# Optimization experiments

Measured on AMD Instinct MI355X. Metric: run time of the kernel, lower is better.

Reference implementation:

```python
import jax, jax.numpy as jnp
import numpy as np
import math

DIM = 2048
NUM_HEADS = 16
HEAD_DIM = DIM // NUM_HEADS
SEQ = 2048
BATCH = 4
THETA = 10000.0


def _rope_tables(seq_len, d, theta):
    # faithful to RotaryEmbedding: emb = cat([freqs, freqs], -1), then [..., ::2]
    inv_freq = 1.0 / theta ** (np.arange(0, d, 2, dtype=np.float32) / d)  # [d/2]
    t = np.arange(seq_len, dtype=np.float32)
    freqs = np.einsum('i,j->ij', t, inv_freq)          # [S, d/2]
    emb = np.concatenate([freqs, freqs], axis=-1)       # [S, d]
    cos_split = np.cos(emb)[:, ::2]                     # [S, d/2]
    sin_split = np.sin(emb)[:, ::2]                     # [S, d/2]
    return jnp.asarray(cos_split), jnp.asarray(sin_split)


def _apply_rope(x, cos_s, sin_s):
    # x: [b, h, s, d]; cos_s/sin_s: [s, d/2]
    x1 = x[..., ::2]
    x2 = x[..., 1::2]
    c = cos_s[None, None]
    s = sin_s[None, None]
    return jnp.concatenate([x1 * c - x2 * s, x1 * s + x2 * c], axis=-1)


def setup_inputs() -> dict:
    key = jax.random.key(0)
    k1, k2, k3 = jax.random.split(key, 3)
    x = jax.random.normal(k1, (BATCH, SEQ, DIM), dtype=jnp.float32)
    # causal additive mask [1,1,S,S]
    neg = jnp.finfo(jnp.float32).min
    causal = jnp.tril(jnp.ones((SEQ, SEQ), dtype=bool))
    mask = jnp.where(causal, 0.0, neg)[None, None].astype(jnp.float32)
    w_qkv = jax.random.normal(k2, (3 * DIM, DIM), dtype=jnp.float32) * (1.0 / math.sqrt(DIM))
    w_out = jax.random.normal(k3, (DIM, DIM), dtype=jnp.float32) * (1.0 / math.sqrt(DIM))
    return {"x": x, "mask": mask, "w_qkv": w_qkv, "w_out": w_out}


def reference(x, mask, w_qkv, w_out):
    b, s, _ = x.shape
    h, d = NUM_HEADS, HEAD_DIM
    qkv = jnp.einsum('bse,fe->bsf', x, w_qkv)           # [b, s, 3*dim]
    q, k, v = jnp.split(qkv, 3, axis=-1)
    # b s (h d) -> b h s d
    reshp = lambda t: t.reshape(b, s, h, d).transpose(0, 2, 1, 3)
    q, k, v = reshp(q), reshp(k), reshp(v)
    cos_s, sin_s = _rope_tables(s, d, THETA)
    q = _apply_rope(q, cos_s, sin_s)
    k = _apply_rope(k, cos_s, sin_s)
    att = jnp.einsum('bhqd,bhkd->bhqk', q, k) / math.sqrt(d)
    att = att + mask
    att = jax.nn.softmax(att, axis=-1)
    y = jnp.einsum('bhqk,bhkd->bhqd', att, v)           # [b, h, s, d]
    y = y.transpose(0, 2, 1, 3).reshape(b, s, h * d)
    return jnp.einsum('bse,fe->bsf', y, w_out)
```

## Files before the change

kernel.cpp:

```cpp
#include <hip/hip_runtime.h>

typedef unsigned short u16;
typedef unsigned int u32;
typedef __attribute__((ext_vector_type(4))) float f32x4;
typedef __attribute__((ext_vector_type(16))) float f32x16;
typedef __attribute__((ext_vector_type(8))) short bf16x8;
typedef __attribute__((ext_vector_type(4))) float float4v;
typedef __attribute__((ext_vector_type(4))) unsigned short u16x4;
typedef __attribute__((ext_vector_type(8))) unsigned short u16x8;

__device__ __forceinline__ float bf2f(u16 u) { return __uint_as_float(((u32)u) << 16); }
__device__ __forceinline__ u16 f2bf(float f) {
  u32 x = __float_as_uint(f);
  x += 0x7fffu + ((x >> 16) & 1u);
  return (u16)(x >> 16);
}
__device__ __forceinline__ u32 cvtpk(float lo, float hi_) {
  u32 r;
  asm("v_cvt_pk_bf16_f32 %0, %1, %2" : "=v"(r) : "v"(lo), "v"(hi_));
  return r;
}

__device__ __forceinline__ void gll16(const void* g, void* l) {
  __builtin_amdgcn_global_load_lds((const __attribute__((address_space(1))) void*)g,
                                   (__attribute__((address_space(3))) void*)l, 16, 0, 0);
}

#define MFMA_BF16(a, b, c) __builtin_amdgcn_mfma_f32_16x16x32_bf16((a), (b), (c), 0, 0, 0)
#define MFMA32(a, b, c) __builtin_amdgcn_mfma_f32_32x32x16_bf16((a), (b), (c), 0, 0, 0)

#define BARRIER() __builtin_amdgcn_s_barrier()
#define SETP(n) __builtin_amdgcn_s_setprio(n)
#define VMCNT(n) asm volatile("s_waitcnt vmcnt(" #n ")" ::: "memory")

__global__ __launch_bounds__(256) void prep_kernel(const float* __restrict__ x,
                                                   const float* __restrict__ w_qkv,
                                                   const float* __restrict__ w_out,
                                                   u16* __restrict__ xb,
                                                   u16* __restrict__ wqkvb,
                                                   u16* __restrict__ woutb,
                                                   float2* __restrict__ cst) {
  const int tid0 = blockIdx.x * 256 + threadIdx.x;
  const int stride = gridDim.x * 256;
#pragma unroll 1
  for (int i = tid0 * 4; i < 16777216; i += stride * 4) {
    const float4v v = *(const float4v*)(x + i);
    u16x4 o; o[0] = f2bf(v[0]); o[1] = f2bf(v[1]); o[2] = f2bf(v[2]); o[3] = f2bf(v[3]);
    *(u16x4*)(xb + i) = o;
  }
#pragma unroll 1
  for (int i = tid0 * 4; i < 12582912; i += stride * 4) {
    const float4v v = *(const float4v*)(w_qkv + i);
    u16x4 o; o[0] = f2bf(v[0]); o[1] = f2bf(v[1]); o[2] = f2bf(v[2]); o[3] = f2bf(v[3]);
    *(u16x4*)(wqkvb + i) = o;
  }
#pragma unroll 1
  for (int i = tid0 * 4; i < 4194304; i += stride * 4) {
    const float4v v = *(const float4v*)(w_out + i);
    u16x4 o; o[0] = f2bf(v[0]); o[1] = f2bf(v[1]); o[2] = f2bf(v[2]); o[3] = f2bf(v[3]);
    *(u16x4*)(woutb + i) = o;
  }
#pragma unroll 1
  for (int idx = tid0; idx < 131072; idx += stride) {
    const int t = idx >> 6, j = idx & 63;
    const float inv = powf(10000.0f, -(float)(j & 31) * (1.0f / 32.0f));
    const float ang = (float)t * inv;
    cst[idx] = make_float2(cosf(ang), sinf(ang));
  }
}

#define PH_MFMA(MG, NG, BF)                                                      \
  do {                                                                           \
    _Pragma("unroll") for (int i_ = 0; i_ < 4; ++i_)                             \
      _Pragma("unroll") for (int jn_ = 0; jn_ < 2; ++jn_)                        \
        _Pragma("unroll") for (int ks_ = 0; ks_ < 2; ++ks_)                      \
          acc[(MG) * 4 + i_][(NG) * 2 + jn_] =                                   \
              MFMA_BF16(af[i_][ks_], BF[jn_][ks_],                               \
                        acc[(MG) * 4 + i_][(NG) * 2 + jn_]);                     \
  } while (0)

#define LDB_M(bb, ng, BF)                                                        \
  do {                                                                           \
    const char* base_ = (const char*)&LDS[bb][1][ng][0];                         \
    _Pragma("unroll") for (int jn_ = 0; jn_ < 2; ++jn_) {                        \
      const int R_ = jn_ * 64 + wc * 16 + l15;                                   \
      _Pragma("unroll") for (int ks_ = 0; ks_ < 2; ++ks_)                        \
        BF[jn_][ks_] = *(const bf16x8*)(base_ + R_ * 128 +                       \
                                        ((ks_ * 64 + l4 * 16) ^ ((R_ & 7) << 4)));\
    }                                                                            \
  } while (0)

#define KTILE(BB, OB, TT)                                                        \
  do {                                                                           \
    LDA_(BB, 0); LDB_M(BB, 0, bfr0);                                            \
    if ((TT) + 1 < NT) STAGE(OB, 0, 0, (TT) + 1);                                \
    BARRIER(); SETP(1); PH_MFMA(0, 0, bfr0); SETP(0); BARRIER();                 \
    LDB_M(BB, 1, bfr1);                                                          \
    if ((TT) + 2 < NT) STAGE(BB, 1, 0, (TT) + 2);                                \
    BARRIER(); SETP(1); PH_MFMA(0, 1, bfr1); SETP(0); BARRIER();                 \
    LDA_(BB, 1);                                                                 \
    if ((TT) + 2 < NT) STAGE(BB, 1, 1, (TT) + 2);                                \
    BARRIER(); SETP(1); PH_MFMA(1, 1, bfr1); SETP(0); BARRIER();                 \
    if ((TT) + 2 < NT) STAGE(BB, 0, 1, (TT) + 2);                                \
    BARRIER(); SETP(1); PH_MFMA(1, 0, bfr0); SETP(0);                            \
    if ((TT) + 2 < NT) { VMCNT(6); } else { VMCNT(0); }                          \
    BARRIER();                                                                   \
  } while (0)

template <int MODE>
__global__ __launch_bounds__(512, 2) void gemm_bt8(const u16* __restrict__ A,
                                                   const u16* __restrict__ B,
                                                   void* __restrict__ Cv, int M, int N, int K,
                                                   int lda, int ldb, int ldc,
                                                   const float2* __restrict__ cst) {
  __shared__ __align__(16) u16 LDS[2][2][2][128 * 64];
  const int nbn = N >> 8;
  const int nwg = gridDim.x;
  const int wg = (blockIdx.x & 7) * (nwg >> 3) + (blockIdx.x >> 3);
  const int bm = wg / nbn, bn = wg % nbn;
  const int tid = threadIdx.x;
  const int w = tid >> 6, l = tid & 63, l15 = l & 15, l4 = l >> 4;
  const int wr = w >> 2, wc = w & 3;
  const u16* Abase = A + (size_t)bm * 256 * lda;
  const u16* Bbase = B + (size_t)bn * 256 * ldb;
  const int NT = K >> 6;

  f32x4 acc[8][4] = {};
  bf16x8 af[4][2], bfr0[2][2], bfr1[2][2];

  auto STAGE = [&](int buf, int sel, int h, int t) {
    const u16* src = (sel ? Bbase + (size_t)h * 128 * ldb : Abase + (size_t)h * 128 * lda) +
                     t * 64;
    const int ld = sel ? ldb : lda;
    char* dst = (char*)&LDS[buf][sel][h][0];
#pragma unroll
    for (int j = 0; j < 2; ++j) {
      const int o = j * 8192 + tid * 16;
      const int r = o >> 7;
      const int cb = (o & 127) ^ ((r & 7) << 4);
      gll16(src + (size_t)r * ld + (cb >> 1), dst + o);
    }
  };
  auto LDA_ = [&](int bb, int mg) {
    const char* base = (const char*)&LDS[bb][0][mg][0];
#pragma unroll
    for (int i = 0; i < 4; ++i) {
      const int R = i * 32 + wr * 16 + l15;
#pragma unroll
      for (int ks = 0; ks < 2; ++ks)
        af[i][ks] = *(const bf16x8*)(base + R * 128 + ((ks * 64 + l4 * 16) ^ ((R & 7) << 4)));
    }
  };

  STAGE(0, 0, 0, 0); STAGE(0, 1, 0, 0); STAGE(0, 0, 1, 0); STAGE(0, 1, 1, 0);
  STAGE(1, 1, 0, 1); STAGE(1, 1, 1, 1); STAGE(1, 0, 1, 1);
  VMCNT(6);
  BARRIER();

  for (int T = 0; T < NT; T += 2) {
    KTILE(0, 1, T);
    KTILE(1, 0, T + 1);
  }

#pragma unroll
  for (int mf = 0; mf < 8; ++mf) {
    const int mg = mf >> 2, i = mf & 3;
    const int row0 = bm * 256 + mg * 128 + i * 32 + wr * 16 + l4 * 4;
#pragma unroll
    for (int f = 0; f < 4; ++f) {
      const int col = bn * 256 + f * 64 + wc * 16 + l15;
      const f32x4 a = acc[mf][f];
      if (MODE == 0) {
        float* C = (float*)Cv;
#pragma unroll
        for (int r = 0; r < 4; ++r)
          C[(size_t)(row0 + r) * ldc + col] = a[r];
      } else if (bn < 16) {
        u16* C = (u16*)Cv;
        const int hc = (f * 64 + wc * 16 + l15) & 127;
        const int jj = hc >> 1;
        const int odd = hc & 1;
        const int co = (col & ~127) + jj + (odd << 6);
#pragma unroll
        for (int r = 0; r < 4; ++r) {
          const int row = row0 + r;
          const int seq = row & 2047;
          const float v = a[r];
          const float p = __shfl_xor(v, 1);
          const float2 cv = cst[seq * 64 + jj];
          const float res = odd ? (p * cv.y + v * cv.x)
                                : (v * cv.x - p * cv.y);
          C[(size_t)row * 6144 + co] = f2bf(res);
        }
      } else {
        u16* C = (u16*)Cv;
        const int batch = row0 >> 11;
        const int s0 = row0 & 2047;
        const int vcol = col - 4096;
        u16* vb = C + (size_t)((batch * 16 + (vcol >> 7)) * 128 + (vcol & 127)) * 6144 +
                  4096 + s0;
        union { u32 u[2]; u16x4 v; } pk;
        pk.u[0] = cvtpk(a[0], a[1]);
        pk.u[1] = cvtpk(a[2], a[3]);
        *(u16x4*)vb = pk.v;
      }
    }
  }
}

__global__ __launch_bounds__(512, 2) void flash_attn(u16* __restrict__ qkvb) {
  __shared__ __align__(16) char smem[65536];
  const int bh = blockIdx.x;
  const int qt = 7 - blockIdx.y;
  const int b = bh >> 4, h = bh & 15;
  const int tid = threadIdx.x;
  const int w = tid >> 6, l = tid & 63;
  const int l31 = l & 31, hi = l >> 5;

  const int q0 = qt * 256 + w * 32;
  const int qg = q0 + l31;

  bf16x8 qf[8];
  {
    const u16* Qrow = qkvb + (size_t)(b * 2048 + qg) * 6144 + h * 128 + hi * 8;
#pragma unroll
    for (int d = 0; d < 8; ++d) qf[d] = *(const bf16x8*)(Qrow + d * 16);
  }

  f32x16 ot[4];
#pragma unroll
  for (int dt = 0; dt < 4; ++dt) ot[dt] = 0.f;
  float mrun = -1e30f, lrun = 0.f;

  const int NT = 4 * qt + 4;
  const u16* Kg0 = qkvb + (size_t)b * 2048 * 6144 + 2048 + h * 128;
  const u16* Vg0 = qkvb + (size_t)bh * 128 * 6144 + 4096;

  auto STAGE = [&](int t) {
    const u16* Kg = Kg0 + (size_t)t * 64 * 6144;
    const u16* Vg = Vg0 + t * 64;
    char* kd = smem + (t & 1) * 16384;
    char* vd = smem + 32768 + (t & 1) * 16384;
#pragma unroll
    for (int j = 0; j < 2; ++j) {
      const int o = j * 8192 + tid * 16;
      {
        const int r = o >> 8;
        const int cb = (o & 255) ^ ((r & 15) << 4);
        gll16(Kg + (size_t)r * 6144 + (cb >> 1), kd + o);
      }
      {
        const int r = o >> 7;
        const int cb = (o & 127) ^ ((r & 7) << 4);
        gll16(Vg + (size_t)r * 6144 + (cb >> 1), vd + o);
      }
    }
  };

  STAGE(0);
  VMCNT(0);
  BARRIER();

  for (int kt = 0; kt < NT; ++kt) {
    if (kt + 1 < NT) STAGE(kt + 1);

    if (kt * 64 <= q0 + 31) {
      const char* Kb = smem + (kt & 1) * 16384;
      const char* Vb = smem + 32768 + (kt & 1) * 16384;

      f32x16 sa[2];
      sa[0] = 0.f; sa[1] = 0.f;
#pragma unroll
      for (int ks2 = 0; ks2 < 2; ++ks2) {
        const int R = ks2 * 32 + l31;
#pragma unroll
        for (int d = 0; d < 8; ++d) {
          const bf16x8 kf = *(const bf16x8*)(Kb + R * 256 +
                                             ((d * 32 + hi * 16) ^ ((R & 15) << 4)));
          sa[ks2] = MFMA32(kf, qf[d], sa[ks2]);
        }
      }

      const float SCALE = 0.08838834764831845f;
      float tmax = -1e30f;
      if (kt * 64 + 63 > q0) {
#pragma unroll
        for (int ks2 = 0; ks2 < 2; ++ks2)
#pragma unroll
          for (int rg = 0; rg < 16; ++rg) {
            const int key = kt * 64 + ks2 * 32 + (rg & 3) + 8 * (rg >> 2) + 4 * hi;
            float sv = sa[ks2][rg] * SCALE;
            sv = (key > qg) ? -1e30f : sv;
            sa[ks2][rg] = sv;
            tmax = fmaxf(tmax, sv);
          }
      } else {
#pragma unroll
        for (int ks2 = 0; ks2 < 2; ++ks2)
#pragma unroll
          for (int rg = 0; rg < 16; ++rg) {
            const float sv = sa[ks2][rg] * SCALE;
            sa[ks2][rg] = sv;
            tmax = fmaxf(tmax, sv);
          }
      }
      tmax = fmaxf(tmax, __shfl_xor(tmax, 32));

      const float mnew = fmaxf(mrun, tmax);
      const float alpha = __expf(mrun - mnew);
      mrun = mnew;
      float rsum = 0.f;
#pragma unroll
      for (int ks2 = 0; ks2 < 2; ++ks2)
#pragma unroll
        for (int rg = 0; rg < 16; ++rg) {
          const float pv = __expf(sa[ks2][rg] - mnew);
          sa[ks2][rg] = pv;
          rsum += pv;
        }
      rsum += __shfl_xor(rsum, 32);
      lrun = lrun * alpha + rsum;
#pragma unroll
      for (int dt = 0; dt < 4; ++dt)
#pragma unroll
        for (int rg = 0; rg < 16; ++rg) ot[dt][rg] *= alpha;

      bf16x8 pfrag[4];
#pragma unroll
      for (int t = 0; t < 4; ++t) {
        const int ks2 = t >> 1;
        const int gA = 2 * (t & 1);
        const int gB = gA + 1;
        const u32 a0 = cvtpk(sa[ks2][gA * 4 + 0], sa[ks2][gA * 4 + 1]);
        const u32 a1 = cvtpk(sa[ks2][gA * 4 + 2], sa[ks2][gA * 4 + 3]);
        const u32 b0 = cvtpk(sa[ks2][gB * 4 + 0], sa[ks2][gB * 4 + 1]);
        const u32 b1 = cvtpk(sa[ks2][gB * 4 + 2], sa[ks2][gB * 4 + 3]);
        const u32 snd0 = hi ? a0 : b0;
        const u32 snd1 = hi ? a1 : b1;
        const u32 rcv0 = (u32)__shfl_xor((int)snd0, 32);
        const u32 rcv1 = (u32)__shfl_xor((int)snd1, 32);
        union { u32 u[4]; bf16x8 v; } pk;
        pk.u[0] = hi ? rcv0 : a0;
        pk.u[1] = hi ? rcv1 : a1;
        pk.u[2] = hi ? b0 : rcv0;
        pk.u[3] = hi ? b1 : rcv1;
        pfrag[t] = pk.v;
      }

#pragma unroll
      for (int dt = 0; dt < 4; ++dt) {
        const int R = dt * 32 + l31;
#pragma unroll
        for (int t = 0; t < 4; ++t) {
          const bf16x8 vf = *(const bf16x8*)(Vb + R * 128 +
                                             ((t * 32 + hi * 16) ^ ((R & 7) << 4)));
          ot[dt] = MFMA32(vf, pfrag[t], ot[dt]);
        }
      }
    }

    VMCNT(0);
    BARRIER();
  }

  const float inv = 1.0f / lrun;
  char* E = smem + w * 8192;
#pragma unroll
  for (int dt = 0; dt < 4; ++dt)
#pragma unroll
    for (int rp = 0; rp < 8; ++rp) {
      const int rg = 2 * rp;
      const int d0 = dt * 32 + (rg & 3) + 8 * (rg >> 2) + 4 * hi;
      const u32 pkv = cvtpk(ot[dt][rg] * inv, ot[dt][rg + 1] * inv);
      *(u32*)(E + l31 * 256 + ((d0 * 2) ^ ((l31 & 15) << 4))) = pkv;
    }
#pragma unroll
  for (int p = 0; p < 8; ++p) {
    const int q = p * 4 + (l >> 4);
    const int c = l & 15;
    const bf16x8 vv = *(const bf16x8*)(E + q * 256 + ((c * 16) ^ ((q & 15) << 4)));
    *(bf16x8*)(qkvb + (size_t)(b * 2048 + q0 + q) * 6144 + h * 128 + c * 8) = vv;
  }
}

extern "C" void kernel_launch(void* const* d_in, const int* in_sizes, int n_in,
                              void* d_out, int out_size, void* d_ws, size_t ws_size,
                              hipStream_t stream) {
  const float* x     = (const float*)d_in[0];
  const float* w_qkv = (const float*)d_in[2];
  const float* w_out = (const float*)d_in[3];
  float* out = (float*)d_out;
  char* ws = (char*)d_ws;

  u16* woutb = (u16*)(ws);
  u16* xb    = (u16*)(ws + ((size_t)8 << 20));
  u16* wqkvb = (u16*)(ws + ((size_t)40 << 20));
  u16* qkvb  = (u16*)(ws + ((size_t)64 << 20));
  float2* cst = (float2*)(ws + ((size_t)160 << 20));

  prep_kernel<<<2048, 256, 0, stream>>>(x, w_qkv, w_out, xb, wqkvb, woutb, cst);
  gemm_bt8<1><<<768, 512, 0, stream>>>(xb, wqkvb, qkvb, 8192, 6144, 2048,
                                       2048, 2048, 6144, cst);
  flash_attn<<<dim3(64, 8), 512, 0, stream>>>(qkvb);
  gemm_bt8<0><<<256, 512, 0, stream>>>(qkvb, woutb, out, 8192, 2048, 2048,
                                       6144, 2048, 2048, nullptr);
}
```

Measured before the change: 411.8 us.

## Restructure GEMM K-tile into two halves with all B fragments loaded once

The 256x256 GEMM K-tile loop changes from four quarter phases (each loading a B sub-fragment and staging one 128-row slab) to two half phases. All four B fragments are loaded into registers up front. Each half runs 32 MFMAs over one A half, and two slabs are staged per half. This halves the number of barriers per K-tile and reduces LDS re-reads of B fragments. In exchange it holds more B fragment registers live, coarsens the overlap between global-to-LDS prefetch and compute, and changes the prologue and wait counts.

```diff
diff --git a/kernel.cpp b/kernel.cpp
--- a/kernel.cpp
+++ b/kernel.cpp
@@ -69,41 +69,35 @@
   }
 }
 
-#define PH_MFMA(MG, NG, BF)                                                      \
+#define PH_HALF(MG)                                                              \
   do {                                                                           \
     _Pragma("unroll") for (int i_ = 0; i_ < 4; ++i_)                             \
-      _Pragma("unroll") for (int jn_ = 0; jn_ < 2; ++jn_)                        \
+      _Pragma("unroll") for (int f_ = 0; f_ < 4; ++f_)                           \
         _Pragma("unroll") for (int ks_ = 0; ks_ < 2; ++ks_)                      \
-          acc[(MG) * 4 + i_][(NG) * 2 + jn_] =                                   \
-              MFMA_BF16(af[i_][ks_], BF[jn_][ks_],                               \
-                        acc[(MG) * 4 + i_][(NG) * 2 + jn_]);                     \
+          acc[(MG) * 4 + i_][f_] =                                               \
+              MFMA_BF16(af[i_][ks_], bfA[f_][ks_], acc[(MG) * 4 + i_][f_]);      \
   } while (0)
 
-#define LDB_M(bb, ng, BF)                                                        \
+#define LDB_ALLM(bb)                                                             \
   do {                                                                           \
-    const char* base_ = (const char*)&LDS[bb][1][ng][0];                         \
-    _Pragma("unroll") for (int jn_ = 0; jn_ < 2; ++jn_) {                        \
-      const int R_ = jn_ * 64 + wc * 16 + l15;                                   \
+    _Pragma("unroll") for (int f_ = 0; f_ < 4; ++f_) {                           \
+      const char* base_ = (const char*)&LDS[bb][1][f_ >> 1][0];                  \
+      const int R_ = (f_ & 1) * 64 + wc * 16 + l15;                              \
       _Pragma("unroll") for (int ks_ = 0; ks_ < 2; ++ks_)                        \
-        BF[jn_][ks_] = *(const bf16x8*)(base_ + R_ * 128 +                       \
+        bfA[f_][ks_] = *(const bf16x8*)(base_ + R_ * 128 +                       \
                                         ((ks_ * 64 + l4 * 16) ^ ((R_ & 7) << 4)));\
     }                                                                            \
   } while (0)
 
-#define KTILE(BB, OB, TT)                                                        \
+#define KTILE2(BB, OB, TT)                                                       \
   do {                                                                           \
-    LDA_(BB, 0); LDB_M(BB, 0, bfr0);                                            \
-    if ((TT) + 1 < NT) STAGE(OB, 0, 0, (TT) + 1);                                \
-    BARRIER(); SETP(1); PH_MFMA(0, 0, bfr0); SETP(0); BARRIER();                 \
-    LDB_M(BB, 1, bfr1);                                                          \
-    if ((TT) + 2 < NT) STAGE(BB, 1, 0, (TT) + 2);                                \
-    BARRIER(); SETP(1); PH_MFMA(0, 1, bfr1); SETP(0); BARRIER();                 \
+    LDA_(BB, 0); LDB_ALLM(BB);                                                  \
+    if ((TT) + 1 < NT) { STAGE(OB, 0, 0, (TT) + 1); STAGE(OB, 0, 1, (TT) + 1); } \
+    BARRIER(); SETP(1); PH_HALF(0); SETP(0); BARRIER();                          \
     LDA_(BB, 1);                                                                 \
-    if ((TT) + 2 < NT) STAGE(BB, 1, 1, (TT) + 2);                                \
-    BARRIER(); SETP(1); PH_MFMA(1, 1, bfr1); SETP(0); BARRIER();                 \
-    if ((TT) + 2 < NT) STAGE(BB, 0, 1, (TT) + 2);                                \
-    BARRIER(); SETP(1); PH_MFMA(1, 0, bfr0); SETP(0);                            \
-    if ((TT) + 2 < NT) { VMCNT(6); } else { VMCNT(0); }                          \
+    if ((TT) + 2 < NT) { STAGE(BB, 1, 0, (TT) + 2); STAGE(BB, 1, 1, (TT) + 2); } \
+    BARRIER(); SETP(1); PH_HALF(1); SETP(0);                                     \
+    if ((TT) + 2 < NT) { VMCNT(4); } else { VMCNT(0); }                          \
     BARRIER();                                                                   \
   } while (0)
 
@@ -126,7 +120,7 @@
   const int NT = K >> 6;
 
   f32x4 acc[8][4] = {};
-  bf16x8 af[4][2], bfr0[2][2], bfr1[2][2];
+  bf16x8 af[4][2], bfA[4][2];
 
   auto STAGE = [&](int buf, int sel, int h, int t) {
     const u16* src = (sel ? Bbase + (size_t)h * 128 * ldb : Abase + (size_t)h * 128 * lda) +
@@ -152,14 +146,13 @@
     }
   };
 
-  STAGE(0, 0, 0, 0); STAGE(0, 1, 0, 0); STAGE(0, 0, 1, 0); STAGE(0, 1, 1, 0);
-  STAGE(1, 1, 0, 1); STAGE(1, 1, 1, 1); STAGE(1, 0, 1, 1);
-  VMCNT(6);
+  STAGE(0, 0, 0, 0); STAGE(0, 0, 1, 0); STAGE(0, 1, 0, 0); STAGE(0, 1, 1, 0);
+  if (NT > 1) { STAGE(1, 1, 0, 1); STAGE(1, 1, 1, 1); VMCNT(4); } else { VMCNT(0); }
   BARRIER();
 
   for (int T = 0; T < NT; T += 2) {
-    KTILE(0, 1, T);
-    KTILE(1, 0, T + 1);
+    KTILE2(0, 1, T);
+    KTILE2(1, 0, T + 1);
   }
 
 #pragma unroll
```

New measurement: 413.7 us. No clear change (+0.4%).

## Triple-buffer K/V in flash attention and add lazy softmax rescaling

Applied to the files above, without the earlier changes.

The attention kernel moves from double to triple buffering of K/V tiles in LDS (grown to 96KB) and prefetches two tiles ahead with a partial vmcnt wait, so loads overlap more compute. The online softmax now rescales the running max and accumulators only when some lane's new max exceeds the old one by more than 8, skipping the exp and the 64 multiplies per tile most of the time. The GEMM K loop is rewritten from a two-step unrolled macro into a single loop indexing buffers by T&1, which may change code generation. The larger LDS footprint can reduce occupancy, and the lazy rescale allows unnormalized exponentials up to e^8, which is within fp32 range.

```diff
diff --git a/kernel.cpp b/kernel.cpp
--- a/kernel.cpp
+++ b/kernel.cpp
@@ -88,23 +88,6 @@
         BF[jn_][ks_] = *(const bf16x8*)(base_ + R_ * 128 +                       \
                                         ((ks_ * 64 + l4 * 16) ^ ((R_ & 7) << 4)));\
     }                                                                            \
-  } while (0)
-
-#define KTILE(BB, OB, TT)                                                        \
-  do {                                                                           \
-    LDA_(BB, 0); LDB_M(BB, 0, bfr0);                                            \
-    if ((TT) + 1 < NT) STAGE(OB, 0, 0, (TT) + 1);                                \
-    BARRIER(); SETP(1); PH_MFMA(0, 0, bfr0); SETP(0); BARRIER();                 \
-    LDB_M(BB, 1, bfr1);                                                          \
-    if ((TT) + 2 < NT) STAGE(BB, 1, 0, (TT) + 2);                                \
-    BARRIER(); SETP(1); PH_MFMA(0, 1, bfr1); SETP(0); BARRIER();                 \
-    LDA_(BB, 1);                                                                 \
-    if ((TT) + 2 < NT) STAGE(BB, 1, 1, (TT) + 2);                                \
-    BARRIER(); SETP(1); PH_MFMA(1, 1, bfr1); SETP(0); BARRIER();                 \
-    if ((TT) + 2 < NT) STAGE(BB, 0, 1, (TT) + 2);                                \
-    BARRIER(); SETP(1); PH_MFMA(1, 0, bfr0); SETP(0);                            \
-    if ((TT) + 2 < NT) { VMCNT(6); } else { VMCNT(0); }                          \
-    BARRIER();                                                                   \
   } while (0)
 
 template <int MODE>
@@ -128,11 +111,11 @@
   f32x4 acc[8][4] = {};
   bf16x8 af[4][2], bfr0[2][2], bfr1[2][2];
 
-  auto STAGE = [&](int buf, int sel, int h, int t) {
+  auto STAGE = [&](int sel, int h, int t) {
     const u16* src = (sel ? Bbase + (size_t)h * 128 * ldb : Abase + (size_t)h * 128 * lda) +
                      t * 64;
     const int ld = sel ? ldb : lda;
-    char* dst = (char*)&LDS[buf][sel][h][0];
+    char* dst = (char*)&LDS[t & 1][sel][h][0];
 #pragma unroll
     for (int j = 0; j < 2; ++j) {
       const int o = j * 8192 + tid * 16;
@@ -152,14 +135,33 @@
     }
   };
 
-  STAGE(0, 0, 0, 0); STAGE(0, 1, 0, 0); STAGE(0, 0, 1, 0); STAGE(0, 1, 1, 0);
-  STAGE(1, 1, 0, 1); STAGE(1, 1, 1, 1); STAGE(1, 0, 1, 1);
+  STAGE(0, 0, 0); STAGE(1, 0, 0); STAGE(0, 1, 0); STAGE(1, 1, 0);
+  if (NT > 1) { STAGE(1, 0, 1); STAGE(1, 1, 1); STAGE(0, 1, 1); }
   VMCNT(6);
   BARRIER();
 
-  for (int T = 0; T < NT; T += 2) {
-    KTILE(0, 1, T);
-    KTILE(1, 0, T + 1);
+  for (int T = 0; T < NT; ++T) {
+    const int bb = T & 1;
+    LDA_(bb, 0); LDB_M(bb, 0, bfr0);
+    if (T + 1 < NT) STAGE(0, 0, T + 1);
+    BARRIER();
+    SETP(1); PH_MFMA(0, 0, bfr0); SETP(0);
+    BARRIER();
+    LDB_M(bb, 1, bfr1);
+    if (T + 2 < NT) STAGE(1, 0, T + 2);
+    BARRIER();
+    SETP(1); PH_MFMA(0, 1, bfr1); SETP(0);
+    BARRIER();
+    LDA_(bb, 1);
+    if (T + 2 < NT) STAGE(1, 1, T + 2);
+    BARRIER();
+    SETP(1); PH_MFMA(1, 1, bfr1); SETP(0);
+    BARRIER();
+    if (T + 2 < NT) STAGE(0, 1, T + 2);
+    BARRIER();
+    SETP(1); PH_MFMA(1, 0, bfr0); SETP(0);
+    if (T + 2 < NT) { VMCNT(6); } else { VMCNT(0); }
+    BARRIER();
   }
 
 #pragma unroll
@@ -209,7 +211,7 @@
 }
 
 __global__ __launch_bounds__(512, 2) void flash_attn(u16* __restrict__ qkvb) {
-  __shared__ __align__(16) char smem[65536];
+  __shared__ __align__(16) char smem[98304];
   const int bh = blockIdx.x;
   const int qt = 7 - blockIdx.y;
   const int b = bh >> 4, h = bh & 15;
@@ -236,11 +238,11 @@
   const u16* Kg0 = qkvb + (size_t)b * 2048 * 6144 + 2048 + h * 128;
   const u16* Vg0 = qkvb + (size_t)bh * 128 * 6144 + 4096;
 
-  auto STAGE = [&](int t) {
+  auto STAGE = [&](int t, int bi) {
     const u16* Kg = Kg0 + (size_t)t * 64 * 6144;
     const u16* Vg = Vg0 + t * 64;
-    char* kd = smem + (t & 1) * 16384;
-    char* vd = smem + 32768 + (t & 1) * 16384;
+    char* kd = smem + bi * 16384;
+    char* vd = smem + 49152 + bi * 16384;
 #pragma unroll
     for (int j = 0; j < 2; ++j) {
       const int o = j * 8192 + tid * 16;
@@ -257,16 +259,18 @@
     }
   };
 
-  STAGE(0);
-  VMCNT(0);
+  STAGE(0, 0);
+  if (NT > 1) { STAGE(1, 1); VMCNT(4); } else { VMCNT(0); }
   BARRIER();
 
+  int cur = 0;
   for (int kt = 0; kt < NT; ++kt) {
-    if (kt + 1 < NT) STAGE(kt + 1);
+    const int nxt = (cur == 0) ? 2 : cur - 1;
+    if (kt + 2 < NT) STAGE(kt + 2, nxt);
 
     if (kt * 64 <= q0 + 31) {
-      const char* Kb = smem + (kt & 1) * 16384;
-      const char* Vb = smem + 32768 + (kt & 1) * 16384;
+      const char* Kb = smem + cur * 16384;
+      const char* Vb = smem + 49152 + cur * 16384;
 
       f32x16 sa[2];
       sa[0] = 0.f; sa[1] = 0.f;
@@ -306,24 +310,27 @@
       }
       tmax = fmaxf(tmax, __shfl_xor(tmax, 32));
 
-      const float mnew = fmaxf(mrun, tmax);
-      const float alpha = __expf(mrun - mnew);
-      mrun = mnew;
+      if (!__all(tmax - mrun <= 8.0f)) {
+        const float mnew = fmaxf(mrun, tmax);
+        const float alpha = __expf(mrun - mnew);
+        mrun = mnew;
+        lrun *= alpha;
+#pragma unroll
+        for (int dt = 0; dt < 4; ++dt)
+#pragma unroll
+          for (int rg = 0; rg < 16; ++rg) ot[dt][rg] *= alpha;
+      }
       float rsum = 0.f;
 #pragma unroll
       for (int ks2 = 0; ks2 < 2; ++ks2)
 #pragma unroll
         for (int rg = 0; rg < 16; ++rg) {
-          const float pv = __expf(sa[ks2][rg] - mnew);
+          const float pv = __expf(sa[ks2][rg] - mrun);
           sa[ks2][rg] = pv;
           rsum += pv;
         }
       rsum += __shfl_xor(rsum, 32);
-      lrun = lrun * alpha + rsum;
-#pragma unroll
-      for (int dt = 0; dt < 4; ++dt)
-#pragma unroll
-        for (int rg = 0; rg < 16; ++rg) ot[dt][rg] *= alpha;
+      lrun += rsum;
 
       bf16x8 pfrag[4];
 #pragma unroll
@@ -359,8 +366,9 @@
       }
     }
 
-    VMCNT(0);
-    BARRIER();
+    if (kt + 2 < NT) { VMCNT(4); } else { VMCNT(0); }
+    BARRIER();
+    cur = (cur == 2) ? 0 : cur + 1;
   }
 
   const float inv = 1.0f / lrun;
```

Measured after the change: 411.2 us. About the same (-0.1%).
